# Kernel tuning notes

Measured on AMD Instinct MI355X. Metric: run time of the kernel, lower is better.

## Reference

```python
import jax, jax.numpy as jnp
import numpy as np

TEMPERATURES = (0.02, 0.05, 0.2)
NORMALIZE_FEATURES = True
NORMALIZE_DRIFT = True
EPS = 1e-8


def _sqdist(a, b):
    # ||a_i - b_j||^2 via expansion; clamp tiny negatives from fp error
    aa = jnp.sum(a * a, axis=1)[:, None]
    bb = jnp.sum(b * b, axis=1)[None, :]
    return jnp.maximum(aa + bb - 2.0 * (a @ b.T), 0.0)


def compute_drifting_field(x, y_pos, y_neg, temperatures):
    """Multi-scale RBF-kernel drifting field.

    V(x) = mean_tau [ softmax_j(-d(x,y_pos_j)/tau) @ y_pos
                    - softmax_k(-d(x,y_neg_k)/tau) @ y_neg ]
    (the attraction/repulsion (y - x) terms: the -x cancels between pos and neg)
    Returns (V, raw_drift_norm, lambda_V).
    """
    D = x.shape[1]
    if NORMALIZE_FEATURES:
        # scale-invariant distances: global RMS of the reference samples
        ref = jnp.concatenate([y_pos, y_neg], axis=0)
        scale = jnp.sqrt(jnp.mean(ref * ref) + EPS)
    else:
        scale = jnp.asarray(1.0, x.dtype)
    xs, yp, yn = x / scale, y_pos / scale, y_neg / scale

    d_pos = _sqdist(xs, yp)  # [N, N_pos]
    d_neg = _sqdist(xs, yn)  # [N, N_neg]

    V = jnp.zeros_like(xs)
    for tau in temperatures:
        w_pos = jax.nn.softmax(-d_pos / tau, axis=1)
        w_neg = jax.nn.softmax(-d_neg / tau, axis=1)
        V = V + (w_pos @ yp - w_neg @ yn)
    V = (V / len(temperatures)) * scale  # back to original feature scale

    raw_drift_norm = jnp.mean(jnp.sum(V * V, axis=1))  # E[||V_raw||^2]
    lambda_V = jnp.sqrt(raw_drift_norm / D + EPS)
    if NORMALIZE_DRIFT:
        V = V / lambda_V
    return V, raw_drift_norm, lambda_V


def reference(x, y_pos, y_neg):
    V, raw_drift_norm, lambda_V = compute_drifting_field(x, y_pos, y_neg, TEMPERATURES)
    x_target = jax.lax.stop_gradient(x + V)
    loss_per_sample = jnp.mean((x - x_target) ** 2, axis=1)
    loss = jnp.mean(loss_per_sample)  # reduction='mean'
    drift_norm = jnp.mean(jnp.sum(V * V, axis=1))
    # per-temperature logging: original redundantly recomputes the full field
    per_temp = jnp.stack([
        compute_drifting_field(x, y_pos, y_neg, (tau,))[1] for tau in TEMPERATURES
    ])
    return loss, drift_norm, raw_drift_norm, lambda_V, per_temp, jax.lax.stop_gradient(V)


def setup_inputs() -> dict:
    key = jax.random.key(0)
    k1, k2, k3 = jax.random.split(key, 3)
    N, D = 4096, 256
    return {
        "x": jax.random.normal(k1, (N, D), dtype=jnp.float32),
        "y_pos": jax.random.normal(k2, (N, D), dtype=jnp.float32),
        "y_neg": jax.random.normal(k3, (N, D), dtype=jnp.float32),
    }
```

## Files before the change

kernel.cpp:

```cpp
#include <hip/hip_runtime.h>

#define NPTS 4096
#define DIM  256
#define TIL  64
#define WCAND 32

typedef unsigned short u16;
typedef unsigned long long u64;
typedef __attribute__((ext_vector_type(8))) short bf16x8;
typedef __attribute__((ext_vector_type(4))) float f32x4;
typedef __attribute__((ext_vector_type(4))) unsigned short u16x4;

__device__ __forceinline__ float exp2fast(float x) {
  float r;
  asm("v_exp_f32 %0, %1" : "=v"(r) : "v"(x));
  return r;
}

__device__ __forceinline__ void gload_lds16(const void* g, void* l) {
  __builtin_amdgcn_global_load_lds((const __attribute__((address_space(1))) void*)g,
                                   (__attribute__((address_space(3))) void*)l, 16, 0, 0);
}

__device__ __forceinline__ float blk_sum4(float v, float* sh) {
  #pragma unroll
  for (int off = 32; off; off >>= 1) v += __shfl_down(v, off);
  int lane = threadIdx.x & 63, w = threadIdx.x >> 6;
  __syncthreads();
  if (lane == 0) sh[w] = v;
  __syncthreads();
  return sh[0] + sh[1] + sh[2] + sh[3];
}

__device__ __forceinline__ float block_scalesq(
    const float* __restrict__ bbp, const float* __restrict__ bbn, float* red, int tid) {
  float s = 0.f;
  #pragma unroll
  for (int q = 0; q < 4; ++q) {
    f32x4 a = *reinterpret_cast<const f32x4*>(bbp + (q * 256 + tid) * 4);
    f32x4 b = *reinterpret_cast<const f32x4*>(bbn + (q * 256 + tid) * 4);
    s += a[0] + a[1] + a[2] + a[3] + b[0] + b[1] + b[2] + b[3];
  }
  float tot = blk_sum4(s, red);
  return tot * (1.0f / (2.0f * NPTS * DIM)) + 1e-8f;
}

__global__ __launch_bounds__(256) void split3_kernel(
    const float* __restrict__ x, const float* __restrict__ yp, const float* __restrict__ yn,
    u16* __restrict__ xb, u16* __restrict__ ypb, u16* __restrict__ ynb,
    float* __restrict__ bbp, float* __restrict__ bbn)
{
  const float* src; u16* dst; float* bb;
  if      (blockIdx.y == 0) { src = x;  dst = xb;  bb = nullptr; }
  else if (blockIdx.y == 1) { src = yp; dst = ypb; bb = bbp; }
  else                      { src = yn; dst = ynb; bb = bbn; }

  int lane = threadIdx.x & 63;
  int wave = threadIdx.x >> 6;
  int row  = blockIdx.x * 4 + wave;
  const float4 v = *reinterpret_cast<const float4*>(src + (size_t)row * DIM + lane * 4);
  float xs[4] = {v.x, v.y, v.z, v.w};
  u16x4 h;
  float ss = 0.f;
  #pragma unroll
  for (int e = 0; e < 4; ++e) {
    unsigned b = __float_as_uint(xs[e]);
    h[e] = (u16)((b + 0x7fffu + ((b >> 16) & 1u)) >> 16);
    ss += xs[e] * xs[e];
  }
  *reinterpret_cast<u16x4*>(dst + (size_t)row * DIM + lane * 4) = h;
  if (bb) {
    #pragma unroll
    for (int off = 32; off; off >>= 1) ss += __shfl_down(ss, off);
    if (lane == 0) bb[row] = ss;
  }
}

__global__ __launch_bounds__(256, 5) void gemm_kernel(
    const u16* __restrict__ Xb, const u16* __restrict__ Ypb, const u16* __restrict__ Ynb,
    const float* __restrict__ bbp, const float* __restrict__ bbn,
    float* __restrict__ M, u64* __restrict__ Kmask)
{
  __shared__ u16 Ah[2][128 * 32];
  __shared__ u16 Bh[2][128 * 32];
  __shared__ float red[4];

  const int tid  = threadIdx.x;

  const unsigned lid = blockIdx.x + (blockIdx.y << 5) + (blockIdx.z << 10);
  const unsigned swz = (lid & 7) * 256 + (lid >> 3);
  const int bx = swz & 31, by = (swz >> 5) & 31, side = (int)(swz >> 10);

  const u16* Yb = side ? Ynb : Ypb;
  const float* bbv = side ? bbn : bbp;

  const int lane = tid & 63;
  const int wave = tid >> 6;
  const int wm = wave >> 1, wn = wave & 1;
  const int l15 = lane & 15, lhi = lane >> 4;

  const int rf = bx * 128;
  const int cf = by * 128;
  const int til = by * 2 + wn;

  const int r0  = tid >> 2;
  const int r1  = 64 + (tid >> 2);
  const int pc  = tid & 3;
  const int gc0 = (pc ^ ((r0 >> 1) & 3)) * 8;
  const int gc1 = (pc ^ ((r1 >> 1) & 3)) * 8;

  const u16* xa0 = Xb + (size_t)(rf + r0) * DIM + gc0;
  const u16* xa1 = Xb + (size_t)(rf + r1) * DIM + gc1;
  const u16* ya0 = Yb + (size_t)(cf + r0) * DIM + gc0;
  const u16* ya1 = Yb + (size_t)(cf + r1) * DIM + gc1;

  f32x4 acc[4][4] = {};

#define STAGE(KS, BUF)                                                 \
  do {                                                                 \
    gload_lds16(xa0 + (KS) * 32, Ah[BUF] + r0 * 32 + pc * 8);          \
    gload_lds16(ya0 + (KS) * 32, Bh[BUF] + r0 * 32 + pc * 8);          \
    gload_lds16(xa1 + (KS) * 32, Ah[BUF] + r1 * 32 + pc * 8);          \
    gload_lds16(ya1 + (KS) * 32, Bh[BUF] + r1 * 32 + pc * 8);          \
  } while (0)

  STAGE(0, 0);

  #pragma unroll
  for (int ks = 0; ks < 8; ++ks) {
    const int cur = ks & 1;
    __builtin_amdgcn_s_barrier();
    if (ks < 7) {
      STAGE(ks + 1, cur ^ 1);
      asm volatile("s_waitcnt vmcnt(4)" ::: "memory");
    } else {
      asm volatile("s_waitcnt vmcnt(0)" ::: "memory");
    }
    __builtin_amdgcn_sched_barrier(0);

    bf16x8 a[4], b[4];
    #pragma unroll
    for (int mi = 0; mi < 4; ++mi) {
      int R = wm * 64 + mi * 16 + l15;
      a[mi] = *reinterpret_cast<const bf16x8*>(Ah[cur] + R * 32 + ((lhi ^ ((R >> 1) & 3)) * 8));
    }
    #pragma unroll
    for (int ni = 0; ni < 4; ++ni) {
      int R = wn * 64 + ni * 16 + l15;
      b[ni] = *reinterpret_cast<const bf16x8*>(Bh[cur] + R * 32 + ((lhi ^ ((R >> 1) & 3)) * 8));
    }
    #pragma unroll
    for (int mi = 0; mi < 4; ++mi)
      #pragma unroll
      for (int ni = 0; ni < 4; ++ni)
        acc[mi][ni] = __builtin_amdgcn_mfma_f32_16x16x32_bf16(a[mi], b[ni], acc[mi][ni], 0, 0, 0);
  }
#undef STAGE

  const float scalesq = block_scalesq(bbp, bbn, red, tid);
  const float thrP = 30.0f * scalesq * 0.2f + 2.5f * scalesq + 0.5f;

  float bbc[4];
  #pragma unroll
  for (int ni = 0; ni < 4; ++ni) bbc[ni] = bbv[cf + wn * 64 + ni * 16 + l15];

  #pragma unroll
  for (int mi = 0; mi < 4; ++mi)
    #pragma unroll
    for (int r = 0; r < 4; ++r) {
      float uv[4];
      float mx = -3.0e38f;
      #pragma unroll
      for (int ni = 0; ni < 4; ++ni) {
        uv[ni] = 2.0f * acc[mi][ni][r] - bbc[ni];
        mx = fmaxf(mx, uv[ni]);
      }
      #pragma unroll
      for (int off = 1; off < 16; off <<= 1) mx = fmaxf(mx, __shfl_xor(mx, off));
      const float cut = mx - thrP;

      u64 bal[4];
      #pragma unroll
      for (int ni = 0; ni < 4; ++ni) bal[ni] = __ballot(uv[ni] > cut);

      u64 mask = 0;
      #pragma unroll
      for (int ni = 0; ni < 4; ++ni)
        mask |= ((bal[ni] >> (lhi * 16)) & 0xFFFFull) << (ni * 16);

      const int rowG = rf + wm * 64 + mi * 16 + lhi * 4 + r;
      if (l15 == 0) {
        Kmask[((size_t)side * NPTS + rowG) * TIL + til] = mask;
        M[((size_t)side * NPTS + rowG) * TIL + til] = mx;
      }
    }
}

__global__ __launch_bounds__(256) void row_kernel(
    const float* __restrict__ M, const u64* __restrict__ Kmask,
    const float* __restrict__ bbp, const float* __restrict__ bbn,
    const float* __restrict__ x,
    const float* __restrict__ ypos, const float* __restrict__ yneg,
    float* __restrict__ parts, float* __restrict__ Vout)
{
  __shared__ unsigned cl[4][2][WCAND];
  __shared__ float red[4];

  const int tid  = threadIdx.x;
  const int lane = tid & 63;
  const int w    = tid >> 6;
  const int row  = blockIdx.x * 4 + w;

  float Mv[2]; u64 km[2];
  #pragma unroll
  for (int side = 0; side < 2; ++side) {
    Mv[side] = M[((size_t)side * NPTS + row) * TIL + lane];
    km[side] = Kmask[((size_t)side * NPTS + row) * TIL + lane];
  }
  const f32x4 xv = *reinterpret_cast<const f32x4*>(x + (size_t)row * DIM + lane * 4);

  const float scalesq = block_scalesq(bbp, bbn, red, tid);
  const float L2E = 1.4426950408889634f;
  const float c0 = L2E / (scalesq * 0.02f);
  const float c1 = L2E / (scalesq * 0.05f);
  const float c2 = L2E / (scalesq * 0.2f);
  const float thrP = 30.0f * scalesq * 0.2f + 2.5f * scalesq + 0.5f;

  int ncs[2];
  #pragma unroll
  for (int side = 0; side < 2; ++side) {
    float g = Mv[side];
    #pragma unroll
    for (int off = 32; off; off >>= 1) g = fmaxf(g, __shfl_xor(g, off));
    u64 mk = (Mv[side] > g - thrP) ? km[side] : 0ull;
    int mycnt = __popcll(mk);
    int pfx = mycnt;
    #pragma unroll
    for (int off = 1; off < 64; off <<= 1) {
      int t = __shfl_up(pfx, off);
      if (lane >= off) pfx += t;
    }
    int base = pfx - mycnt;
    int nc = __shfl(pfx, 63);
    u64 b = mk;
    int s = base;
    while (b) {
      int bit = __ffsll((long long)b) - 1;
      b &= b - 1;
      if (s < WCAND) cl[w][side][s] = lane * 64 + bit;
      ++s;
    }
    ncs[side] = nc < WCAND ? nc : WCAND;
  }

  f32x4 V0 = {0,0,0,0}, V1 = {0,0,0,0}, V2 = {0,0,0,0};

  for (int side = 0; side < 2; ++side) {
    const float* bb = side ? bbn : bbp;
    const float* y  = side ? yneg : ypos;
    const float sgn = side ? -1.f : 1.f;
    const int nc = ncs[side];

    float me = -3.0e38f, p0 = 0.f, p1 = 0.f, p2 = 0.f;
    f32x4 A0 = {0,0,0,0}, A1 = {0,0,0,0}, A2 = {0,0,0,0};
    for (int bs = 0; bs < nc; bs += 8) {
      const int rem = nc - bs;
      int jq[8];
      f32x4 yv[8];
      float dq[8], uq[8];
      #pragma unroll
      for (int q = 0; q < 8; ++q) {
        int idx = (q < rem) ? bs + q : bs;
        jq[q] = (int)cl[w][side][idx];
        yv[q] = *reinterpret_cast<const f32x4*>(y + (size_t)jq[q] * DIM + lane * 4);
      }
      #pragma unroll
      for (int q = 0; q < 8; ++q)
        dq[q] = xv[0]*yv[q][0] + xv[1]*yv[q][1] + xv[2]*yv[q][2] + xv[3]*yv[q][3];
      #pragma unroll
      for (int off = 32; off; off >>= 1)
        #pragma unroll
        for (int q = 0; q < 8; ++q) dq[q] += __shfl_xor(dq[q], off);
      #pragma unroll
      for (int q = 0; q < 8; ++q)
        uq[q] = (q < rem) ? 2.0f * dq[q] - bb[jq[q]] : -3.0e38f;

      float cm = uq[0];
      #pragma unroll
      for (int q = 1; q < 8; ++q) cm = fmaxf(cm, uq[q]);
      float nm = fmaxf(me, cm);
      float s0 = exp2fast((me - nm) * c0);
      float s1 = exp2fast((me - nm) * c1);
      float s2 = exp2fast((me - nm) * c2);
      p0 *= s0; p1 *= s1; p2 *= s2;
      A0 *= s0; A1 *= s1; A2 *= s2;
      #pragma unroll
      for (int q = 0; q < 8; ++q) {
        float du = uq[q] - nm;
        float e0 = exp2fast(du * c0);
        float e1 = exp2fast(du * c1);
        float e2 = exp2fast(du * c2);
        p0 += e0; p1 += e1; p2 += e2;
        A0 += e0 * yv[q]; A1 += e1 * yv[q]; A2 += e2 * yv[q];
      }
      me = nm;
    }
    V0 += (sgn / p0) * A0;
    V1 += (sgn / p1) * A1;
    V2 += (sgn / p2) * A2;
  }

  f32x4 vr = (V0 + V1 + V2) * (1.0f / 3.0f);
  *reinterpret_cast<f32x4*>(Vout + (size_t)row * DIM + lane * 4) = vr;

  float s0 = V0[0]*V0[0] + V0[1]*V0[1] + V0[2]*V0[2] + V0[3]*V0[3];
  float s1 = V1[0]*V1[0] + V1[1]*V1[1] + V1[2]*V1[2] + V1[3]*V1[3];
  float s2 = V2[0]*V2[0] + V2[1]*V2[1] + V2[2]*V2[2] + V2[3]*V2[3];
  float sr = vr[0]*vr[0] + vr[1]*vr[1] + vr[2]*vr[2] + vr[3]*vr[3];
  #pragma unroll
  for (int off = 32; off; off >>= 1) {
    s0 += __shfl_xor(s0, off);
    s1 += __shfl_xor(s1, off);
    s2 += __shfl_xor(s2, off);
    sr += __shfl_xor(sr, off);
  }
  if (lane == 0) {
    parts[row]            = sr;
    parts[NPTS + row]     = s0;
    parts[2 * NPTS + row] = s1;
    parts[3 * NPTS + row] = s2;
  }
}

__global__ __launch_bounds__(256) void final_kernel(
    const float* __restrict__ parts, float* __restrict__ out)
{
  __shared__ float red[4];
  const int tid = threadIdx.x;

  float s = 0.f;
  for (int k = tid; k < NPTS; k += 256) s += parts[k];
  float raw = blk_sum4(s, red) * (1.0f / NPTS);
  float lam2 = raw * (1.0f / DIM) + 1e-8f;
  float lam  = sqrtf(lam2);
  float inv  = 1.0f / lam;

  int idx = blockIdx.x * 256 + tid;
  out[7 + idx] *= inv;

  if (blockIdx.x == 0) {
    #pragma unroll
    for (int a = 1; a <= 3; ++a) {
      float t = 0.f;
      for (int k = tid; k < NPTS; k += 256) t += parts[a * NPTS + k];
      t = blk_sum4(t, red);
      if (tid == 0) out[3 + a] = t * (1.0f / NPTS);
    }
    if (tid == 0) {
      float drift = raw / lam2;
      out[0] = drift * (1.0f / DIM);
      out[1] = drift;
      out[2] = raw;
      out[3] = lam;
    }
  }
}

extern "C" void kernel_launch(void* const* d_in, const int* in_sizes, int n_in,
                              void* d_out, int out_size, void* d_ws, size_t ws_size,
                              hipStream_t stream)
{
  (void)in_sizes; (void)n_in; (void)out_size; (void)ws_size;
  const float* x    = (const float*)d_in[0];
  const float* ypos = (const float*)d_in[1];
  const float* yneg = (const float*)d_in[2];
  float* out = (float*)d_out;
  char* ws = (char*)d_ws;

  float* bbp   = (float*)ws;
  float* bbn   = (float*)(ws + 16384);
  float* parts = (float*)(ws + 32768);
  float* M     = (float*)(ws + 98304);
  u64*   Kmask = (u64*)(ws + 98304 + 2097152);
  u16* xb  = (u16*)(ws + 98304 + 2097152 + 4194304);
  u16* ypb = xb + (size_t)NPTS * DIM;
  u16* ynb = xb + 2 * (size_t)NPTS * DIM;

  split3_kernel<<<dim3(NPTS / 4, 3), 256, 0, stream>>>(x, ypos, yneg, xb, ypb, ynb, bbp, bbn);
  gemm_kernel<<<dim3(32, 32, 2), 256, 0, stream>>>(xb, ypb, ynb, bbp, bbn, M, Kmask);
  row_kernel<<<NPTS / 4, 256, 0, stream>>>(M, Kmask, bbp, bbn, x, ypos, yneg,
                                           parts, out + 7);
  final_kernel<<<NPTS, 256, 0, stream>>>(parts, out);
}
```

Baseline: 77.75 us.

## Compute positive and negative distance tiles in one block sharing the X tile

Merges the two side-specific GEMM blocks into one block that loads the X tile once and multiplies it against both y_pos and y_neg tiles, keeping two accumulator sets. This halves X tile global/LDS traffic and halves the grid size. In exchange, register use doubles (accumulators 128 VGPRs), the occupancy hint is dropped, LDS per block grows, and there are fewer blocks (1024) to fill the GPU.

```diff
diff --git a/kernel.cpp b/kernel.cpp
--- a/kernel.cpp
+++ b/kernel.cpp
@@ -76,23 +76,21 @@
   }
 }
 
-__global__ __launch_bounds__(256, 5) void gemm_kernel(
+__global__ __launch_bounds__(256) void gemm_kernel(
     const u16* __restrict__ Xb, const u16* __restrict__ Ypb, const u16* __restrict__ Ynb,
     const float* __restrict__ bbp, const float* __restrict__ bbn,
     float* __restrict__ M, u64* __restrict__ Kmask)
 {
   __shared__ u16 Ah[2][128 * 32];
-  __shared__ u16 Bh[2][128 * 32];
+  __shared__ u16 Bp[2][128 * 32];
+  __shared__ u16 Bn[2][128 * 32];
   __shared__ float red[4];
 
   const int tid  = threadIdx.x;
 
-  const unsigned lid = blockIdx.x + (blockIdx.y << 5) + (blockIdx.z << 10);
-  const unsigned swz = (lid & 7) * 256 + (lid >> 3);
-  const int bx = swz & 31, by = (swz >> 5) & 31, side = (int)(swz >> 10);
-
-  const u16* Yb = side ? Ynb : Ypb;
-  const float* bbv = side ? bbn : bbp;
+  const unsigned lid = blockIdx.x + (blockIdx.y << 5);
+  const unsigned swz = (lid & 7) * 128 + (lid >> 3);
+  const int bx = swz & 31, by = (int)(swz >> 5);
 
   const int lane = tid & 63;
   const int wave = tid >> 6;
@@ -109,19 +107,24 @@
   const int gc0 = (pc ^ ((r0 >> 1) & 3)) * 8;
   const int gc1 = (pc ^ ((r1 >> 1) & 3)) * 8;
 
-  const u16* xa0 = Xb + (size_t)(rf + r0) * DIM + gc0;
-  const u16* xa1 = Xb + (size_t)(rf + r1) * DIM + gc1;
-  const u16* ya0 = Yb + (size_t)(cf + r0) * DIM + gc0;
-  const u16* ya1 = Yb + (size_t)(cf + r1) * DIM + gc1;
-
-  f32x4 acc[4][4] = {};
+  const u16* xa0 = Xb  + (size_t)(rf + r0) * DIM + gc0;
+  const u16* xa1 = Xb  + (size_t)(rf + r1) * DIM + gc1;
+  const u16* yp0 = Ypb + (size_t)(cf + r0) * DIM + gc0;
+  const u16* yp1 = Ypb + (size_t)(cf + r1) * DIM + gc1;
+  const u16* yn0 = Ynb + (size_t)(cf + r0) * DIM + gc0;
+  const u16* yn1 = Ynb + (size_t)(cf + r1) * DIM + gc1;
+
+  f32x4 accP[4][4] = {};
+  f32x4 accN[4][4] = {};
 
 #define STAGE(KS, BUF)                                                 \
   do {                                                                 \
     gload_lds16(xa0 + (KS) * 32, Ah[BUF] + r0 * 32 + pc * 8);          \
-    gload_lds16(ya0 + (KS) * 32, Bh[BUF] + r0 * 32 + pc * 8);          \
+    gload_lds16(yp0 + (KS) * 32, Bp[BUF] + r0 * 32 + pc * 8);          \
+    gload_lds16(yn0 + (KS) * 32, Bn[BUF] + r0 * 32 + pc * 8);          \
     gload_lds16(xa1 + (KS) * 32, Ah[BUF] + r1 * 32 + pc * 8);          \
-    gload_lds16(ya1 + (KS) * 32, Bh[BUF] + r1 * 32 + pc * 8);          \
+    gload_lds16(yp1 + (KS) * 32, Bp[BUF] + r1 * 32 + pc * 8);          \
+    gload_lds16(yn1 + (KS) * 32, Bn[BUF] + r1 * 32 + pc * 8);          \
   } while (0)
 
   STAGE(0, 0);
@@ -132,13 +135,13 @@
     __builtin_amdgcn_s_barrier();
     if (ks < 7) {
       STAGE(ks + 1, cur ^ 1);
-      asm volatile("s_waitcnt vmcnt(4)" ::: "memory");
+      asm volatile("s_waitcnt vmcnt(6)" ::: "memory");
     } else {
       asm volatile("s_waitcnt vmcnt(0)" ::: "memory");
     }
     __builtin_amdgcn_sched_barrier(0);
 
-    bf16x8 a[4], b[4];
+    bf16x8 a[4], bp[4], bn[4];
     #pragma unroll
     for (int mi = 0; mi < 4; ++mi) {
       int R = wm * 64 + mi * 16 + l15;
@@ -147,53 +150,59 @@
     #pragma unroll
     for (int ni = 0; ni < 4; ++ni) {
       int R = wn * 64 + ni * 16 + l15;
-      b[ni] = *reinterpret_cast<const bf16x8*>(Bh[cur] + R * 32 + ((lhi ^ ((R >> 1) & 3)) * 8));
+      int off = R * 32 + ((lhi ^ ((R >> 1) & 3)) * 8);
+      bp[ni] = *reinterpret_cast<const bf16x8*>(Bp[cur] + off);
+      bn[ni] = *reinterpret_cast<const bf16x8*>(Bn[cur] + off);
     }
     #pragma unroll
     for (int mi = 0; mi < 4; ++mi)
       #pragma unroll
-      for (int ni = 0; ni < 4; ++ni)
-        acc[mi][ni] = __builtin_amdgcn_mfma_f32_16x16x32_bf16(a[mi], b[ni], acc[mi][ni], 0, 0, 0);
+      for (int ni = 0; ni < 4; ++ni) {
+        accP[mi][ni] = __builtin_amdgcn_mfma_f32_16x16x32_bf16(a[mi], bp[ni], accP[mi][ni], 0, 0, 0);
+        accN[mi][ni] = __builtin_amdgcn_mfma_f32_16x16x32_bf16(a[mi], bn[ni], accN[mi][ni], 0, 0, 0);
+      }
   }
 #undef STAGE
 
   const float scalesq = block_scalesq(bbp, bbn, red, tid);
   const float thrP = 30.0f * scalesq * 0.2f + 2.5f * scalesq + 0.5f;
 
-  float bbc[4];
-  #pragma unroll
-  for (int ni = 0; ni < 4; ++ni) bbc[ni] = bbv[cf + wn * 64 + ni * 16 + l15];
-
-  #pragma unroll
-  for (int mi = 0; mi < 4; ++mi)
-    #pragma unroll
-    for (int r = 0; r < 4; ++r) {
-      float uv[4];
-      float mx = -3.0e38f;
-      #pragma unroll
-      for (int ni = 0; ni < 4; ++ni) {
-        uv[ni] = 2.0f * acc[mi][ni][r] - bbc[ni];
-        mx = fmaxf(mx, uv[ni]);
-      }
-      #pragma unroll
-      for (int off = 1; off < 16; off <<= 1) mx = fmaxf(mx, __shfl_xor(mx, off));
-      const float cut = mx - thrP;
-
-      u64 bal[4];
-      #pragma unroll
-      for (int ni = 0; ni < 4; ++ni) bal[ni] = __ballot(uv[ni] > cut);
-
-      u64 mask = 0;
-      #pragma unroll
-      for (int ni = 0; ni < 4; ++ni)
-        mask |= ((bal[ni] >> (lhi * 16)) & 0xFFFFull) << (ni * 16);
-
-      const int rowG = rf + wm * 64 + mi * 16 + lhi * 4 + r;
-      if (l15 == 0) {
-        Kmask[((size_t)side * NPTS + rowG) * TIL + til] = mask;
-        M[((size_t)side * NPTS + rowG) * TIL + til] = mx;
-      }
-    }
+#define EMIT(ACC, BBV, SIDE)                                                     \
+  do {                                                                           \
+    float bbc[4];                                                                \
+    _Pragma("unroll")                                                            \
+    for (int ni = 0; ni < 4; ++ni) bbc[ni] = (BBV)[cf + wn * 64 + ni * 16 + l15];\
+    _Pragma("unroll")                                                            \
+    for (int mi = 0; mi < 4; ++mi)                                               \
+      _Pragma("unroll")                                                          \
+      for (int r = 0; r < 4; ++r) {                                              \
+        float uv[4];                                                             \
+        float mx = -3.0e38f;                                                     \
+        _Pragma("unroll")                                                        \
+        for (int ni = 0; ni < 4; ++ni) {                                         \
+          uv[ni] = 2.0f * (ACC)[mi][ni][r] - bbc[ni];                            \
+          mx = fmaxf(mx, uv[ni]);                                                \
+        }                                                                        \
+        _Pragma("unroll")                                                        \
+        for (int off = 1; off < 16; off <<= 1) mx = fmaxf(mx, __shfl_xor(mx, off)); \
+        const float cut = mx - thrP;                                             \
+        u64 mask = 0;                                                            \
+        _Pragma("unroll")                                                        \
+        for (int ni = 0; ni < 4; ++ni) {                                         \
+          u64 bal = __ballot(uv[ni] > cut);                                      \
+          mask |= ((bal >> (lhi * 16)) & 0xFFFFull) << (ni * 16);                \
+        }                                                                        \
+        const int rowG = rf + wm * 64 + mi * 16 + lhi * 4 + r;                   \
+        if (l15 == 0) {                                                          \
+          Kmask[((size_t)(SIDE) * NPTS + rowG) * TIL + til] = mask;              \
+          M[((size_t)(SIDE) * NPTS + rowG) * TIL + til] = mx;                    \
+        }                                                                        \
+      }                                                                          \
+  } while (0)
+
+  EMIT(accP, bbp, 0);
+  EMIT(accN, bbn, 1);
+#undef EMIT
 }
 
 __global__ __launch_bounds__(256) void row_kernel(
@@ -387,7 +396,7 @@
   u16* ynb = xb + 2 * (size_t)NPTS * DIM;
 
   split3_kernel<<<dim3(NPTS / 4, 3), 256, 0, stream>>>(x, ypos, yneg, xb, ypb, ynb, bbp, bbn);
-  gemm_kernel<<<dim3(32, 32, 2), 256, 0, stream>>>(xb, ypb, ynb, bbp, bbn, M, Kmask);
+  gemm_kernel<<<dim3(32, 32), 256, 0, stream>>>(xb, ypb, ynb, bbp, bbn, M, Kmask);
   row_kernel<<<NPTS / 4, 256, 0, stream>>>(M, Kmask, bbp, bbn, x, ypos, yneg,
                                            parts, out + 7);
   final_kernel<<<NPTS, 256, 0, stream>>>(parts, out);
```

Result: slower. 101.4 us (+30.4%).
